# Kernel optimization log

Measured on AMD Instinct MI355X. Metric: run time of the kernel, lower is better.

## Reference

```python
import jax, jax.numpy as jnp
import numpy as np

LIGAND_W = 1.0
SIDECHAIN_W = 0.5
LIGAND_DIST_W = 0.2
SIDECHAIN_DIST_W = 0.1
CUTOFF = 5.0
EPS = 1e-12


def _pdist(x):
    # x: [..., N, 3] -> (dist [..., N, N], sq [..., N, N]); safe sqrt for grads
    d = x[..., :, None, :] - x[..., None, :, :]
    sq = jnp.sum(d * d, axis=-1)
    return jnp.sqrt(jnp.maximum(sq, EPS)), sq


def _masked_dist_loss(pred, tgt, valid):
    # pred/tgt: [..., N, 3], valid: [..., N] float. Returns (per-group loss, has-any flag)
    pd, _ = _pdist(pred)
    td, tsq = _pdist(tgt)
    pair = valid[..., :, None] * valid[..., None, :]
    dmask = pair * (tsq > 0.0).astype(pred.dtype) * (td <= CUTOFF).astype(pred.dtype)
    num = jnp.sum(dmask * (pd - td) ** 2, axis=(-1, -2))
    den = jnp.sum(dmask, axis=(-1, -2))
    return num / jnp.maximum(den, 1.0), den > 0.0


def setup_inputs() -> dict:
    key = jax.random.key(0)
    k1, k2, k3, k4, k5, k6 = jax.random.split(key, 6)
    B, L, R, A = 64, 512, 1024, 14
    ligand_tgt = jax.random.normal(k2, (B, L, 3), dtype=jnp.float32) * 3.0
    ligand_pred = ligand_tgt + 0.5 * jax.random.normal(k1, (B, L, 3), dtype=jnp.float32)
    sidechain_tgt = jax.random.normal(k4, (B, R, A, 3), dtype=jnp.float32) * 2.0
    sidechain_pred = sidechain_tgt + 0.5 * jax.random.normal(k3, (B, R, A, 3), dtype=jnp.float32)
    ligand_mask = jax.random.bernoulli(k5, 0.9, (B, L))
    atom_mask = jax.random.bernoulli(k6, 0.7, (B, R, A))
    return {
        'ligand_pred': ligand_pred, 'ligand_tgt': ligand_tgt,
        'sidechain_pred': sidechain_pred, 'sidechain_tgt': sidechain_tgt,
        'ligand_mask': ligand_mask, 'atom_mask': atom_mask,
    }


def reference(ligand_pred, ligand_tgt, sidechain_pred, sidechain_tgt, ligand_mask, atom_mask):
    f = ligand_pred.dtype
    lm = ligand_mask.astype(f)              # [B, L]
    am = atom_mask.astype(f)                # [B, R, A]

    # --- ligand coord loss: per-batch mse (mean over valid atoms * 3), then mean over batches ---
    se = jnp.sum((ligand_pred - ligand_tgt) ** 2, axis=-1) * lm   # [B, L]
    lig_cnt = jnp.sum(lm, axis=-1)                                # [B]
    ligand_loss = jnp.mean(jnp.sum(se, axis=-1) / (3.0 * jnp.maximum(lig_cnt, 1.0)))

    # --- ligand distance-preservation loss ---
    lig_d, lig_has = _masked_dist_loss(ligand_pred, ligand_tgt, lm)  # [B], [B]
    ligand_dist_loss = jnp.sum(jnp.where(lig_has, lig_d, 0.0)) / jnp.maximum(jnp.sum(lig_has.astype(f)), 1.0)

    # --- sidechain coord loss: per-atom mse (mean over 3), mean over all valid atoms ---
    atom_mse = jnp.mean((sidechain_pred - sidechain_tgt) ** 2, axis=-1)  # [B, R, A]
    sc_cnt = jnp.sum(am)
    sidechain_loss = jnp.sum(atom_mse * am) / jnp.maximum(sc_cnt, 1.0)

    # --- sidechain distance-preservation loss: per-residue groups ---
    sc_d, sc_has = _masked_dist_loss(sidechain_pred, sidechain_tgt, am)  # [B, R]
    sidechain_dist_loss = jnp.sum(jnp.where(sc_has, sc_d, 0.0)) / jnp.maximum(jnp.sum(sc_has.astype(f)), 1.0)

    total = (LIGAND_W * ligand_loss
             + LIGAND_DIST_W * ligand_dist_loss
             + SIDECHAIN_W * sidechain_loss
             + SIDECHAIN_DIST_W * sidechain_dist_loss)
    return total
```

## Files before the change

### kernel.cpp

```cpp
#include <hip/hip_runtime.h>

#define CUTOFF 5.0f
#define DEPS 1e-12f
#define FSQRT(x) __builtin_amdgcn_sqrtf(x)


#define NSC_BLK 512
#define NLIG_BLK 512
#define GRID (NSC_BLK + NLIG_BLK)

__global__ __launch_bounds__(256) void fused_kernel(
    const float* __restrict__ lig_pred, const float* __restrict__ lig_tgt,
    const int* __restrict__ lig_mask,
    const float* __restrict__ sc_pred, const float* __restrict__ sc_tgt,
    const int* __restrict__ sc_mask,
    float* __restrict__ ws) {
  const int tid = threadIdx.x;
  __shared__ float4 stage4[1344];
  __shared__ float red[4][4];

  if (blockIdx.x < NSC_BLK) {
    const int sb = blockIdx.x;
    float ax[7], ay[7], az[7];
    float bx[7], by[7], bz[7];
    float m[7];

    const float4* srcp = (const float4*)(sc_pred + (size_t)sb * 5376);
    for (int k = tid; k < 1344; k += 256) stage4[k] = srcp[k];
    __syncthreads();
    {
      const float* s = ((const float*)stage4) + tid * 21;
#pragma unroll
      for (int a = 0; a < 7; a++) { ax[a] = s[3 * a]; ay[a] = s[3 * a + 1]; az[a] = s[3 * a + 2]; }
    }
    __syncthreads();
    const float4* srct = (const float4*)(sc_tgt + (size_t)sb * 5376);
    for (int k = tid; k < 1344; k += 256) stage4[k] = srct[k];
    __syncthreads();
    {
      const float* s = ((const float*)stage4) + tid * 21;
#pragma unroll
      for (int a = 0; a < 7; a++) { bx[a] = s[3 * a]; by[a] = s[3 * a + 1]; bz[a] = s[3 * a + 2]; }
    }
    const int* mp = sc_mask + (size_t)sb * 1792 + tid * 7;
#pragma unroll
    for (int a = 0; a < 7; a++) m[a] = (mp[a] != 0) ? 1.f : 0.f;

    float mse = 0.f, am = 0.f;
#pragma unroll
    for (int a = 0; a < 7; a++) {
      float dx = ax[a] - bx[a], dy = ay[a] - by[a], dz = az[a] - bz[a];
      mse += m[a] * ((dx * dx + dy * dy + dz * dz) * (1.f / 3.f));
      am += m[a];
    }

    float num = 0.f, den = 0.f;
#pragma unroll
    for (int js = 0; js < 7; js++) {
#pragma unroll
      for (int side = 0; side < 2; side++) {
        float jx, jy, jz, kx, ky, kz, mj;
        if (side == 0) {
          jx = ax[js]; jy = ay[js]; jz = az[js];
          kx = bx[js]; ky = by[js]; kz = bz[js];
          mj = m[js];
        } else {
          jx = __shfl_xor(ax[js], 1, 64); jy = __shfl_xor(ay[js], 1, 64);
          jz = __shfl_xor(az[js], 1, 64);
          kx = __shfl_xor(bx[js], 1, 64); ky = __shfl_xor(by[js], 1, 64);
          kz = __shfl_xor(bz[js], 1, 64);
          mj = __shfl_xor(m[js], 1, 64);
        }
#pragma unroll
        for (int i = 0; i < 7; i++) {
          float dx = bx[i] - kx, dy = by[i] - ky, dz = bz[i] - kz;
          float tsq = dx * dx + dy * dy + dz * dz;
          float td = FSQRT(fmaxf(tsq, DEPS));
          float w = m[i] * mj;
          w = (tsq > 0.f) ? w : 0.f;
          w = (td <= CUTOFF) ? w : 0.f;
          float qx = ax[i] - jx, qy = ay[i] - jy, qz = az[i] - jz;
          float pd = FSQRT(fmaxf(qx * qx + qy * qy + qz * qz, DEPS));
          float d = pd - td;
          num += w * d * d;
          den += w;
        }
      }
    }
    float num_g = num + __shfl_xor(num, 1, 64);
    float den_g = den + __shfl_xor(den, 1, 64);
    float val = (den_g > 0.f) ? 0.5f * (num_g / fmaxf(den_g, 1.f)) : 0.f;
    float has = (den_g > 0.f) ? 0.5f : 0.f;

    for (int off = 32; off > 0; off >>= 1) {
      mse += __shfl_down(mse, off, 64);
      am += __shfl_down(am, off, 64);
      val += __shfl_down(val, off, 64);
      has += __shfl_down(has, off, 64);
    }
    int lane = tid & 63, wv = tid >> 6;
    if (lane == 0) { red[0][wv] = mse; red[1][wv] = am; red[2][wv] = val; red[3][wv] = has; }
    __syncthreads();
    if (tid == 0) {
      float* p = ws + 1088 + (size_t)sb * 4;
      p[0] = red[0][0] + red[0][1] + red[0][2] + red[0][3];
      p[1] = red[1][0] + red[1][1] + red[1][2] + red[1][3];
      p[2] = red[2][0] + red[2][1] + red[2][2] + red[2][3];
      p[3] = red[3][0] + red[3][1] + red[3][2] + red[3][3];
    }
  } else {
    const int L = 512;
    const int lb = blockIdx.x - NSC_BLK;
    const int b = lb >> 3;
    const int t = lb & 7;
    const int i0a = 32 * t;
    const int i0b = 32 * (15 - t);
    const float* pb = lig_pred + (size_t)b * L * 3;
    const float* tb = lig_tgt + (size_t)b * L * 3;
    const int* mb = lig_mask + (size_t)b * L;

    float4* st4 = stage4;
    float4* sp4 = stage4 + 64;

    if (tid < 128) {
      int which = tid >> 5;
      int idx = tid & 31;
      int i = ((which & 1) ? i0b : i0a) + idx;
      if (which < 2) {
        st4[(which << 5) + idx] =
            make_float4(tb[3 * i], tb[3 * i + 1], tb[3 * i + 2], (mb[i] != 0) ? 1.f : 0.f);
      } else {
        sp4[((which & 1) << 5) + idx] =
            make_float4(pb[3 * i], pb[3 * i + 1], pb[3 * i + 2], 0.f);
      }
    }
    __syncthreads();

    float num0 = 0.f, den0 = 0.f, num1 = 0.f, den1 = 0.f, se = 0.f, cnt = 0.f;

#pragma unroll
    for (int k = 0; k < 2; k++) {
      const int js = i0a + (k << 8) + tid;
      if (js < L) {
        float pjx = pb[3 * js], pjy = pb[3 * js + 1], pjz = pb[3 * js + 2];
        float tjx = tb[3 * js], tjy = tb[3 * js + 1], tjz = tb[3 * js + 2];
        float mj = (mb[js] != 0) ? 1.f : 0.f;
        if (t == 0) {
          float dx = pjx - tjx, dy = pjy - tjy, dz = pjz - tjz;
          se += mj * (dx * dx + dy * dy + dz * dz);
          cnt += mj;
        }
#pragma unroll 4
        for (int ii = 0; ii < 32; ii++) {
          float4 ti = st4[ii];
          float4 pi = sp4[ii];
          float w = (js > i0a + ii) ? ti.w * mj : 0.f;
          float dx = ti.x - tjx, dy = ti.y - tjy, dz = ti.z - tjz;
          float tsq = dx * dx + dy * dy + dz * dz;
          float td = FSQRT(fmaxf(tsq, DEPS));
          w = (tsq > 0.f) ? w : 0.f;
          w = (td <= CUTOFF) ? w : 0.f;
          float qx = pi.x - pjx, qy = pi.y - pjy, qz = pi.z - pjz;
          float pd = FSQRT(fmaxf(qx * qx + qy * qy + qz * qz, DEPS));
          float d = pd - td;
          if (ii & 1) { num1 += w * d * d; den1 += w; }
          else        { num0 += w * d * d; den0 += w; }
        }
      }
    }

    {
      const int js = i0b + tid;
      if (js < L) {
        float pjx = pb[3 * js], pjy = pb[3 * js + 1], pjz = pb[3 * js + 2];
        float tjx = tb[3 * js], tjy = tb[3 * js + 1], tjz = tb[3 * js + 2];
        float mj = (mb[js] != 0) ? 1.f : 0.f;
#pragma unroll 4
        for (int ii = 0; ii < 32; ii++) {
          float4 ti = st4[32 + ii];
          float4 pi = sp4[32 + ii];
          float w = (js > i0b + ii) ? ti.w * mj : 0.f;
          float dx = ti.x - tjx, dy = ti.y - tjy, dz = ti.z - tjz;
          float tsq = dx * dx + dy * dy + dz * dz;
          float td = FSQRT(fmaxf(tsq, DEPS));
          w = (tsq > 0.f) ? w : 0.f;
          w = (td <= CUTOFF) ? w : 0.f;
          float qx = pi.x - pjx, qy = pi.y - pjy, qz = pi.z - pjz;
          float pd = FSQRT(fmaxf(qx * qx + qy * qy + qz * qz, DEPS));
          float d = pd - td;
          if (ii & 1) { num1 += w * d * d; den1 += w; }
          else        { num0 += w * d * d; den0 += w; }
        }
      }
    }

    float num = num0 + num1, den = den0 + den1;
    for (int off = 32; off > 0; off >>= 1) {
      num += __shfl_down(num, off, 64);
      den += __shfl_down(den, off, 64);
      se += __shfl_down(se, off, 64);
      cnt += __shfl_down(cnt, off, 64);
    }
    int lane = tid & 63, wv = tid >> 6;
    if (lane == 0) { red[0][wv] = num; red[1][wv] = den; red[2][wv] = se; red[3][wv] = cnt; }
    __syncthreads();
    if (tid == 0) {
      ws[lb * 2 + 0] = red[0][0] + red[0][1] + red[0][2] + red[0][3];
      ws[lb * 2 + 1] = red[1][0] + red[1][1] + red[1][2] + red[1][3];
      if (t == 0) {
        float se_t = red[2][0] + red[2][1] + red[2][2] + red[2][3];
        float cnt_t = red[3][0] + red[3][1] + red[3][2] + red[3][3];
        ws[1024 + b] = se_t / (3.f * fmaxf(cnt_t, 1.f));
      }
    }
  }
}

__global__ __launch_bounds__(256) void finalize_kernel(const float* __restrict__ ws,
                                                       float* __restrict__ out) {
  const int tid = threadIdx.x;
  __shared__ float sred[4][4];

  const float* sc = ws + 1088;
  float s0 = 0.f, s1 = 0.f, s2 = 0.f, s3 = 0.f;
  for (int i = tid; i < 512; i += 256) {
    s0 += sc[4 * i + 0]; s1 += sc[4 * i + 1]; s2 += sc[4 * i + 2]; s3 += sc[4 * i + 3];
  }
  for (int off = 32; off > 0; off >>= 1) {
    s0 += __shfl_down(s0, off, 64);
    s1 += __shfl_down(s1, off, 64);
    s2 += __shfl_down(s2, off, 64);
    s3 += __shfl_down(s3, off, 64);
  }
  int lane = tid & 63, wv = tid >> 6;
  if (lane == 0) { sred[0][wv] = s0; sred[1][wv] = s1; sred[2][wv] = s2; sred[3][wv] = s3; }
  __syncthreads();

  float lval = 0.f, lhas = 0.f, lcoord = 0.f;
  if (tid < 64) {
    float n = 0.f, d = 0.f;
    for (int t = 0; t < 8; t++) {
      n += ws[(tid * 8 + t) * 2 + 0];
      d += ws[(tid * 8 + t) * 2 + 1];
    }
    lval = (d > 0.f) ? n / fmaxf(d, 1.f) : 0.f;
    lhas = (d > 0.f) ? 1.f : 0.f;
    lcoord = ws[1024 + tid];
    for (int off = 32; off > 0; off >>= 1) {
      lval += __shfl_down(lval, off, 64);
      lhas += __shfl_down(lhas, off, 64);
      lcoord += __shfl_down(lcoord, off, 64);
    }
  }
  if (tid == 0) {
    float sc_mse = sred[0][0] + sred[0][1] + sred[0][2] + sred[0][3];
    float sc_am = sred[1][0] + sred[1][1] + sred[1][2] + sred[1][3];
    float sc_val = sred[2][0] + sred[2][1] + sred[2][2] + sred[2][3];
    float sc_has = sred[3][0] + sred[3][1] + sred[3][2] + sred[3][3];
    float ligand_loss = lcoord * (1.f / 64.f);
    float ligand_dist_loss = lval / fmaxf(lhas, 1.f);
    float sidechain_loss = sc_mse / fmaxf(sc_am, 1.f);
    float sidechain_dist_loss = sc_val / fmaxf(sc_has, 1.f);
    out[0] = ligand_loss + 0.2f * ligand_dist_loss + 0.5f * sidechain_loss +
             0.1f * sidechain_dist_loss;
  }
}

extern "C" void kernel_launch(void* const* d_in, const int* in_sizes, int n_in,
                              void* d_out, int out_size, void* d_ws, size_t ws_size,
                              hipStream_t stream) {
  const float* ligand_pred = (const float*)d_in[0];
  const float* ligand_tgt = (const float*)d_in[1];
  const float* sidechain_pred = (const float*)d_in[2];
  const float* sidechain_tgt = (const float*)d_in[3];
  const int* ligand_mask = (const int*)d_in[4];
  const int* atom_mask = (const int*)d_in[5];
  float* out = (float*)d_out;
  float* ws = (float*)d_ws;

  fused_kernel<<<GRID, 256, 0, stream>>>(ligand_pred, ligand_tgt, ligand_mask,
                                         sidechain_pred, sidechain_tgt, atom_mask, ws);
  finalize_kernel<<<1, 256, 0, stream>>>(ws, out);
}
```

Baseline: 105.7 us.

## Fuse finalize into main kernel via atomics and last-block reduction; drop LDS staging

Removes the separate finalize kernel. Blocks now accumulate partial sums with global atomics, and the last block to finish, detected through an atomic counter, computes the final loss; a memset launch is added to zero the accumulators. The ligand path also stops staging its i-rows in shared memory and instead reads them straight from global memory inside a fully unrolled loop. This trades a kernel launch for a memset plus atomic contention, and the uniform global loads lean on the cache. Float atomics also make the summation order nondeterministic.

```diff
diff --git a/kernel.cpp b/kernel.cpp
--- a/kernel.cpp
+++ b/kernel.cpp
@@ -14,10 +14,15 @@
     const int* __restrict__ lig_mask,
     const float* __restrict__ sc_pred, const float* __restrict__ sc_tgt,
     const int* __restrict__ sc_mask,
-    float* __restrict__ ws) {
+    float* __restrict__ ws, float* __restrict__ out) {
   const int tid = threadIdx.x;
+  float* bnum = ws + 8;
+  float* bden = ws + 72;
+  unsigned int* done = (unsigned int*)(ws + 1);
+
   __shared__ float4 stage4[1344];
   __shared__ float red[4][4];
+  __shared__ bool last;
 
   if (blockIdx.x < NSC_BLK) {
     const int sb = blockIdx.x;
@@ -102,11 +107,10 @@
     if (lane == 0) { red[0][wv] = mse; red[1][wv] = am; red[2][wv] = val; red[3][wv] = has; }
     __syncthreads();
     if (tid == 0) {
-      float* p = ws + 1088 + (size_t)sb * 4;
-      p[0] = red[0][0] + red[0][1] + red[0][2] + red[0][3];
-      p[1] = red[1][0] + red[1][1] + red[1][2] + red[1][3];
-      p[2] = red[2][0] + red[2][1] + red[2][2] + red[2][3];
-      p[3] = red[3][0] + red[3][1] + red[3][2] + red[3][3];
+      atomicAdd(&ws[3], red[0][0] + red[0][1] + red[0][2] + red[0][3]);
+      atomicAdd(&ws[4], red[1][0] + red[1][1] + red[1][2] + red[1][3]);
+      atomicAdd(&ws[5], red[2][0] + red[2][1] + red[2][2] + red[2][3]);
+      atomicAdd(&ws[6], red[3][0] + red[3][1] + red[3][2] + red[3][3]);
     }
   } else {
     const int L = 512;
@@ -119,23 +123,6 @@
     const float* tb = lig_tgt + (size_t)b * L * 3;
     const int* mb = lig_mask + (size_t)b * L;
 
-    float4* st4 = stage4;
-    float4* sp4 = stage4 + 64;
-
-    if (tid < 128) {
-      int which = tid >> 5;
-      int idx = tid & 31;
-      int i = ((which & 1) ? i0b : i0a) + idx;
-      if (which < 2) {
-        st4[(which << 5) + idx] =
-            make_float4(tb[3 * i], tb[3 * i + 1], tb[3 * i + 2], (mb[i] != 0) ? 1.f : 0.f);
-      } else {
-        sp4[((which & 1) << 5) + idx] =
-            make_float4(pb[3 * i], pb[3 * i + 1], pb[3 * i + 2], 0.f);
-      }
-    }
-    __syncthreads();
-
     float num0 = 0.f, den0 = 0.f, num1 = 0.f, den1 = 0.f, se = 0.f, cnt = 0.f;
 
 #pragma unroll
@@ -150,17 +137,19 @@
           se += mj * (dx * dx + dy * dy + dz * dz);
           cnt += mj;
         }
-#pragma unroll 4
+#pragma unroll
         for (int ii = 0; ii < 32; ii++) {
-          float4 ti = st4[ii];
-          float4 pi = sp4[ii];
-          float w = (js > i0a + ii) ? ti.w * mj : 0.f;
-          float dx = ti.x - tjx, dy = ti.y - tjy, dz = ti.z - tjz;
+          const int i = i0a + ii;
+          float tix = tb[3 * i], tiy = tb[3 * i + 1], tiz = tb[3 * i + 2];
+          float pix = pb[3 * i], piy = pb[3 * i + 1], piz = pb[3 * i + 2];
+          float mi = (mb[i] != 0) ? 1.f : 0.f;
+          float w = (js > i) ? mi * mj : 0.f;
+          float dx = tix - tjx, dy = tiy - tjy, dz = tiz - tjz;
           float tsq = dx * dx + dy * dy + dz * dz;
           float td = FSQRT(fmaxf(tsq, DEPS));
           w = (tsq > 0.f) ? w : 0.f;
           w = (td <= CUTOFF) ? w : 0.f;
-          float qx = pi.x - pjx, qy = pi.y - pjy, qz = pi.z - pjz;
+          float qx = pix - pjx, qy = piy - pjy, qz = piz - pjz;
           float pd = FSQRT(fmaxf(qx * qx + qy * qy + qz * qz, DEPS));
           float d = pd - td;
           if (ii & 1) { num1 += w * d * d; den1 += w; }
@@ -175,17 +164,19 @@
         float pjx = pb[3 * js], pjy = pb[3 * js + 1], pjz = pb[3 * js + 2];
         float tjx = tb[3 * js], tjy = tb[3 * js + 1], tjz = tb[3 * js + 2];
         float mj = (mb[js] != 0) ? 1.f : 0.f;
-#pragma unroll 4
+#pragma unroll
         for (int ii = 0; ii < 32; ii++) {
-          float4 ti = st4[32 + ii];
-          float4 pi = sp4[32 + ii];
-          float w = (js > i0b + ii) ? ti.w * mj : 0.f;
-          float dx = ti.x - tjx, dy = ti.y - tjy, dz = ti.z - tjz;
+          const int i = i0b + ii;
+          float tix = tb[3 * i], tiy = tb[3 * i + 1], tiz = tb[3 * i + 2];
+          float pix = pb[3 * i], piy = pb[3 * i + 1], piz = pb[3 * i + 2];
+          float mi = (mb[i] != 0) ? 1.f : 0.f;
+          float w = (js > i) ? mi * mj : 0.f;
+          float dx = tix - tjx, dy = tiy - tjy, dz = tiz - tjz;
           float tsq = dx * dx + dy * dy + dz * dz;
           float td = FSQRT(fmaxf(tsq, DEPS));
           w = (tsq > 0.f) ? w : 0.f;
           w = (td <= CUTOFF) ? w : 0.f;
-          float qx = pi.x - pjx, qy = pi.y - pjy, qz = pi.z - pjz;
+          float qx = pix - pjx, qy = piy - pjy, qz = piz - pjz;
           float pd = FSQRT(fmaxf(qx * qx + qy * qy + qz * qz, DEPS));
           float d = pd - td;
           if (ii & 1) { num1 += w * d * d; den1 += w; }
@@ -205,64 +196,46 @@
     if (lane == 0) { red[0][wv] = num; red[1][wv] = den; red[2][wv] = se; red[3][wv] = cnt; }
     __syncthreads();
     if (tid == 0) {
-      ws[lb * 2 + 0] = red[0][0] + red[0][1] + red[0][2] + red[0][3];
-      ws[lb * 2 + 1] = red[1][0] + red[1][1] + red[1][2] + red[1][3];
+      atomicAdd(&bnum[b], red[0][0] + red[0][1] + red[0][2] + red[0][3]);
+      atomicAdd(&bden[b], red[1][0] + red[1][1] + red[1][2] + red[1][3]);
       if (t == 0) {
         float se_t = red[2][0] + red[2][1] + red[2][2] + red[2][3];
         float cnt_t = red[3][0] + red[3][1] + red[3][2] + red[3][3];
-        ws[1024 + b] = se_t / (3.f * fmaxf(cnt_t, 1.f));
+        atomicAdd(&ws[0], se_t / (3.f * fmaxf(cnt_t, 1.f)));
       }
     }
   }
-}
-
-__global__ __launch_bounds__(256) void finalize_kernel(const float* __restrict__ ws,
-                                                       float* __restrict__ out) {
-  const int tid = threadIdx.x;
-  __shared__ float sred[4][4];
-
-  const float* sc = ws + 1088;
-  float s0 = 0.f, s1 = 0.f, s2 = 0.f, s3 = 0.f;
-  for (int i = tid; i < 512; i += 256) {
-    s0 += sc[4 * i + 0]; s1 += sc[4 * i + 1]; s2 += sc[4 * i + 2]; s3 += sc[4 * i + 3];
+
+  if (tid == 0) {
+    __threadfence();
+    unsigned int old = atomicAdd(done, 1u);
+    last = (old == GRID - 1);
   }
-  for (int off = 32; off > 0; off >>= 1) {
-    s0 += __shfl_down(s0, off, 64);
-    s1 += __shfl_down(s1, off, 64);
-    s2 += __shfl_down(s2, off, 64);
-    s3 += __shfl_down(s3, off, 64);
-  }
-  int lane = tid & 63, wv = tid >> 6;
-  if (lane == 0) { sred[0][wv] = s0; sred[1][wv] = s1; sred[2][wv] = s2; sred[3][wv] = s3; }
   __syncthreads();
-
-  float lval = 0.f, lhas = 0.f, lcoord = 0.f;
-  if (tid < 64) {
-    float n = 0.f, d = 0.f;
-    for (int t = 0; t < 8; t++) {
-      n += ws[(tid * 8 + t) * 2 + 0];
-      d += ws[(tid * 8 + t) * 2 + 1];
-    }
-    lval = (d > 0.f) ? n / fmaxf(d, 1.f) : 0.f;
-    lhas = (d > 0.f) ? 1.f : 0.f;
-    lcoord = ws[1024 + tid];
-    for (int off = 32; off > 0; off >>= 1) {
-      lval += __shfl_down(lval, off, 64);
-      lhas += __shfl_down(lhas, off, 64);
-      lcoord += __shfl_down(lcoord, off, 64);
-    }
-  }
-  if (tid == 0) {
-    float sc_mse = sred[0][0] + sred[0][1] + sred[0][2] + sred[0][3];
-    float sc_am = sred[1][0] + sred[1][1] + sred[1][2] + sred[1][3];
-    float sc_val = sred[2][0] + sred[2][1] + sred[2][2] + sred[2][3];
-    float sc_has = sred[3][0] + sred[3][1] + sred[3][2] + sred[3][3];
-    float ligand_loss = lcoord * (1.f / 64.f);
-    float ligand_dist_loss = lval / fmaxf(lhas, 1.f);
-    float sidechain_loss = sc_mse / fmaxf(sc_am, 1.f);
-    float sidechain_dist_loss = sc_val / fmaxf(sc_has, 1.f);
-    out[0] = ligand_loss + 0.2f * ligand_dist_loss + 0.5f * sidechain_loss +
-             0.1f * sidechain_dist_loss;
+  if (last) {
+    __threadfence();
+    if (tid < 64) {
+      float n = atomicAdd(&bnum[tid], 0.f);
+      float d = atomicAdd(&bden[tid], 0.f);
+      float val = (d > 0.f) ? n / fmaxf(d, 1.f) : 0.f;
+      float has = (d > 0.f) ? 1.f : 0.f;
+      for (int off = 32; off > 0; off >>= 1) {
+        val += __shfl_down(val, off, 64);
+        has += __shfl_down(has, off, 64);
+      }
+      if (tid == 0) {
+        float lig = atomicAdd(&ws[0], 0.f) * (1.f / 64.f);
+        float sc_mse = atomicAdd(&ws[3], 0.f);
+        float sc_am = atomicAdd(&ws[4], 0.f);
+        float sc_val = atomicAdd(&ws[5], 0.f);
+        float sc_has = atomicAdd(&ws[6], 0.f);
+        float ligand_dist_loss = val / fmaxf(has, 1.f);
+        float sidechain_loss = sc_mse / fmaxf(sc_am, 1.f);
+        float sidechain_dist_loss = sc_val / fmaxf(sc_has, 1.f);
+        out[0] = lig + 0.2f * ligand_dist_loss + 0.5f * sidechain_loss +
+                 0.1f * sidechain_dist_loss;
+      }
+    }
   }
 }
 
@@ -278,7 +251,8 @@
   float* out = (float*)d_out;
   float* ws = (float*)d_ws;
 
+  hipMemsetAsync(ws, 0, 136 * sizeof(float), stream);
   fused_kernel<<<GRID, 256, 0, stream>>>(ligand_pred, ligand_tgt, ligand_mask,
-                                         sidechain_pred, sidechain_tgt, atom_mask, ws);
-  finalize_kernel<<<1, 256, 0, stream>>>(ws, out);
+                                         sidechain_pred, sidechain_tgt, atom_mask,
+                                         ws, out);
 }
```

Result: slower. 138.7 us (+31.2%).
